# Kernel optimization log

Hardware: AMD Instinct MI355X
Metric: run time of the kernel (lower is better)

Reference implementation:

```python
import jax, jax.numpy as jnp
import numpy as np

KS = 5               # kernel_size per spline dimension
K3 = KS ** 3         # 125 weight matrices per SplineConv
NS = [16384, 4096, 1024, 256, 64]  # nodes per hierarchy level
DEG = 8


def spline_basis(pseudo):
    """Degree-1 open B-spline basis for 3D pseudo-coords in [0,1].
    Returns basis [E,8] and weight indices [E,8] into the K3 weights."""
    v = pseudo * (KS - 1)
    bot = jnp.minimum(jnp.floor(v), KS - 2)
    frac = v - bot                                  # [E,3]
    bot = bot.astype(jnp.int32)
    bits = jnp.array([[(s >> d) & 1 for d in range(3)] for s in range(8)], jnp.int32)  # [8,3]
    f = frac[:, None, :]                            # [E,1,3]
    basis = jnp.prod(jnp.where(bits[None] == 1, f, 1.0 - f), axis=-1)   # [E,8]
    strides = jnp.array([1, KS, KS * KS], jnp.int32)
    widx = jnp.sum((bot[:, None, :] + bits[None]) * strides, axis=-1)   # [E,8]
    return basis, widx


def spline_conv(x, src, dst, basis, widx, W, root, bias, n):
    """out_j = (1/deg_j) * sum_{i->j} sum_s B_s(u_ij) x_i W_{k(s)} + x_j root + bias.
    Accumulate basis-weighted source features into per-(node, weight-index)
    buckets, then one dense einsum with the 125 kernel weights."""
    in_c = x.shape[1]
    contrib = basis[..., None] * x[src][:, None, :]          # [E,8,in]
    flat = (dst[:, None] * K3 + widx).reshape(-1)            # [E*8]
    acc = jnp.zeros((n * K3, in_c), x.dtype).at[flat].add(contrib.reshape(-1, in_c))
    out = jnp.einsum('nki,kio->no', acc.reshape(n, K3, in_c), W)
    deg = jnp.zeros((n,), x.dtype).at[dst].add(1.0)
    return out / jnp.maximum(deg, 1.0)[:, None] + x @ root + bias


def setup_inputs() -> dict:
    rng = np.random.default_rng(0)
    inp = {}
    inp['x'] = jnp.asarray(rng.standard_normal((NS[0], 1)), jnp.float32)
    for l in range(4):
        e = NS[l] * DEG
        inp[f'src{l}'] = jnp.asarray(rng.integers(0, NS[l], e), jnp.int32)
        inp[f'dst{l}'] = jnp.asarray(rng.integers(0, NS[l], e), jnp.int32)
        inp[f'pseudo{l}'] = jnp.asarray(rng.random((e, 3)), jnp.float32)
        cl = np.arange(NS[l]) % NS[l + 1]  # guarantees every voxel cluster non-empty
        rng.shuffle(cl)
        inp[f'cluster{l}'] = jnp.asarray(cl, jnp.int32)
    chans = [(1, 32), (32, 32), (32, 64), (64, 64), (64, 64), (64, 64), (64, 64), (64, 64)]
    names = ['1', '12', '2', '3', '4', '5', '6', '7']
    for nm, (ci, co) in zip(names, chans):
        inp[f'W{nm}'] = jnp.asarray(rng.standard_normal((K3, ci, co)) / np.sqrt(8.0 * ci), jnp.float32)
        inp[f'R{nm}'] = jnp.asarray(rng.standard_normal((ci, co)) / np.sqrt(ci), jnp.float32)
        inp[f'B{nm}'] = jnp.zeros((co,), jnp.float32)
    inp['fc1_w'] = jnp.asarray(rng.standard_normal((64, 64)) / 8.0, jnp.float32)
    inp['fc1_b'] = jnp.zeros((64,), jnp.float32)
    inp['fc2_w'] = jnp.asarray(rng.standard_normal((64, 10)) / 8.0, jnp.float32)
    inp['fc2_b'] = jnp.zeros((10,), jnp.float32)
    return inp


def reference(x, pseudo0, pseudo1, pseudo2, pseudo3,
              src0, dst0, src1, dst1, src2, dst2, src3, dst3,
              cluster0, cluster1, cluster2, cluster3,
              W1, R1, B1, W12, R12, B12, W2, R2, B2, W3, R3, B3,
              W4, R4, B4, W5, R5, B5, W6, R6, B6, W7, R7, B7,
              fc1_w, fc1_b, fc2_w, fc2_b):
    elu = jax.nn.elu
    # level 0
    b, wi = spline_basis(pseudo0)
    h = elu(spline_conv(x, src0, dst0, b, wi, W1, R1, B1, NS[0]))
    h = elu(spline_conv(h, src0, dst0, b, wi, W12, R12, B12, NS[0]))
    h = jax.ops.segment_max(h, cluster0, num_segments=NS[1])   # voxel max pool 1
    # level 1
    b, wi = spline_basis(pseudo1)
    h = elu(spline_conv(h, src1, dst1, b, wi, W2, R2, B2, NS[1]))
    h = elu(spline_conv(h, src1, dst1, b, wi, W3, R3, B3, NS[1]))
    h = jax.ops.segment_max(h, cluster1, num_segments=NS[2])   # voxel max pool 2
    # level 2
    b, wi = spline_basis(pseudo2)
    h = elu(spline_conv(h, src2, dst2, b, wi, W4, R4, B4, NS[2]))
    h = elu(spline_conv(h, src2, dst2, b, wi, W5, R5, B5, NS[2]))
    h = jax.ops.segment_max(h, cluster2, num_segments=NS[3])   # voxel max pool 3
    # level 3
    b, wi = spline_basis(pseudo3)
    h = elu(spline_conv(h, src3, dst3, b, wi, W6, R6, B6, NS[3]))
    h = elu(spline_conv(h, src3, dst3, b, wi, W7, R7, B7, NS[3]))
    h = jax.ops.segment_max(h, cluster3, num_segments=NS[4])   # voxel max pool 4
    # readout head (dropout is identity in eval mode)
    g = h.mean(0)[None, :]
    g = g @ fc1_w + fc1_b
    g = g @ fc2_w + fc2_b
    return jax.nn.log_softmax(g, axis=1)
```

## Files before the change

### kernel.cpp

```cpp
#include <hip/hip_runtime.h>
#include <hip/hip_bf16.h>

#define KS 5
#define K3 125

typedef __attribute__((ext_vector_type(8))) short short8;
typedef __attribute__((ext_vector_type(4))) float floatx4;

__device__ inline unsigned enc_f(float f) {
    int b = __float_as_int(f);
    return (b >= 0) ? ((unsigned)b | 0x80000000u) : ~((unsigned)b);
}

__device__ inline unsigned short f2bf(float f) {
    unsigned u = __float_as_uint(f);
    u += 0x7FFFu + ((u >> 16) & 1u);
    return (unsigned short)(u >> 16);
}
__device__ inline float bf2f(unsigned short h) {
    return __uint_as_float((unsigned)h << 16);
}
__device__ inline unsigned pack2bf(float a, float b) {
    return (unsigned)f2bf(a) | ((unsigned)f2bf(b) << 16);
}

__device__ inline void edge_basis(const float* __restrict__ pseudo, int e,
                                  float* bs, int* ks) {
    float fr[3];
    int bot[3];
#pragma unroll
    for (int d = 0; d < 3; ++d) {
        float v = pseudo[e * 3 + d] * (float)(KS - 1);
        float fl = fminf(floorf(v), (float)(KS - 2));
        fr[d] = v - fl;
        bot[d] = (int)fl;
    }
    const int strides[3] = {1, KS, KS * KS};
#pragma unroll
    for (int s = 0; s < 8; ++s) {
        float b = 1.f;
        int w = 0;
#pragma unroll
        for (int d = 0; d < 3; ++d) {
            int bit = (s >> d) & 1;
            b *= bit ? fr[d] : (1.f - fr[d]);
            w += (bot[d] + bit) * strides[d];
        }
        bs[s] = b;
        ks[s] = w;
    }
}

__device__ inline void edge_fracs(const float* __restrict__ pseudo, int e, float* bs) {
    float fr[3];
#pragma unroll
    for (int d = 0; d < 3; ++d) {
        float v = pseudo[e * 3 + d] * (float)(KS - 1);
        float fl = fminf(floorf(v), (float)(KS - 2));
        fr[d] = v - fl;
    }
#pragma unroll
    for (int s = 0; s < 8; ++s) {
        float b = 1.f;
#pragma unroll
        for (int d = 0; d < 3; ++d) b *= ((s >> d) & 1) ? fr[d] : (1.f - fr[d]);
        bs[s] = b;
    }
}

__device__ inline int edge_bucket(const float* __restrict__ pseudo, int e) {
    int kb = 0;
#pragma unroll
    for (int d = 0; d < 3; ++d) {
        float v = pseudo[e * 3 + d] * (float)(KS - 1);
        int fl = (int)fminf(floorf(v), (float)(KS - 2));
        kb += fl << (2 * d);
    }
    return kb;
}

__global__ __launch_bounds__(256) void hist_deg_clist_all(
    const float* __restrict__ p0, const float* __restrict__ p1,
    const float* __restrict__ p2, const float* __restrict__ p3,
    const int* __restrict__ d0, const int* __restrict__ d1,
    const int* __restrict__ d2, const int* __restrict__ d3,
    const int* __restrict__ c0, const int* __restrict__ c1,
    const int* __restrict__ c2, const int* __restrict__ c3,
    int* __restrict__ hist, int* __restrict__ degi,
    int* __restrict__ ccnt, int* __restrict__ clist) {
    int b = blockIdx.x;
    if (b >= 680) {
        int idx = (b - 680) * 256 + threadIdx.x;
        int j, cof, nof;
        const int* cl;
        if (idx < 16384)      { j = idx;         cl = c0; cof = 0;    nof = 0; }
        else if (idx < 20480) { j = idx - 16384; cl = c1; cof = 4096; nof = 16384; }
        else if (idx < 21504) { j = idx - 20480; cl = c2; cof = 5120; nof = 20480; }
        else if (idx < 21760) { j = idx - 21504; cl = c3; cof = 5376; nof = 21504; }
        else return;
        int c = cl[j];
        int slot = atomicAdd(&ccnt[cof + c], 1);
        clist[nof + c * 4 + slot] = j;
        return;
    }
    int l, lb, E, dof;
    const float* ps;
    const int* ds;
    if (b < 512)      { l = 0; lb = b;       ps = p0; ds = d0; E = 131072; dof = 0; }
    else if (b < 640) { l = 1; lb = b - 512; ps = p1; ds = d1; E = 32768;  dof = 16384; }
    else if (b < 672) { l = 2; lb = b - 640; ps = p2; ds = d2; E = 8192;   dof = 20480; }
    else              { l = 3; lb = b - 672; ps = p3; ds = d3; E = 2048;   dof = 21504; }
    __shared__ int h[64];
    int t = threadIdx.x;
    if (t < 64) h[t] = 0;
    __syncthreads();
    int e = lb * 256 + t;
    if (e < E) {
        atomicAdd(&h[edge_bucket(ps, e)], 1);
        atomicAdd(&degi[dof + ds[e]], 1);
    }
    __syncthreads();
    if (t < 64 && h[t]) atomicAdd(&hist[l * 64 + t], h[t]);
}

__global__ void scan_pad_all(const int* __restrict__ hist, int* __restrict__ gcur,
                             int* __restrict__ tileOf, int* __restrict__ pack) {
    const int TBv[4] = {0, 2112, 2112 + 576, 2112 + 576 + 192};
    int l = blockIdx.x;
    int tileBase = TBv[l];
    __shared__ int sh[64];
    int t = threadIdx.x;
    int cnt = hist[l * 64 + t];
    int tiles = (cnt + 63) >> 6;
    sh[t] = tiles;
    __syncthreads();
    for (int d = 1; d < 64; d <<= 1) {
        int v = (t >= d) ? sh[t - d] : 0;
        __syncthreads();
        sh[t] += v;
        __syncthreads();
    }
    int tb = tileBase + sh[t] - tiles;
    int eb = tb * 64;
    gcur[l * 64 + t] = eb;
    for (int q = 0; q < tiles; ++q) tileOf[tb + q] = t;
    for (int idx = eb + cnt; idx < eb + tiles * 64; ++idx) pack[idx] = -1;
}

__global__ __launch_bounds__(1024) void csr_scan_all(const int* __restrict__ degi,
                                                     int* __restrict__ off,
                                                     int* __restrict__ cur) {
    const int Nv[4] = {16384, 4096, 1024, 256};
    const int DOFv[4] = {0, 16384, 20480, 21504};
    const int OFFv[4] = {0, 16385, 20482, 21507};
    int l = blockIdx.x;
    int n = Nv[l];
    const int* d = degi + DOFv[l];
    int* o = off + OFFv[l];
    int* c = cur + DOFv[l];
    __shared__ int ls[1024];
    int t = threadIdx.x;
    int per = (n + 1023) >> 10;
    int beg = t * per;
    int end = (beg + per < n) ? beg + per : n;
    int s = 0;
    for (int j = beg; j < end; ++j) s += d[j];
    ls[t] = s;
    __syncthreads();
    for (int dd = 1; dd < 1024; dd <<= 1) {
        int v = (t >= dd) ? ls[t - dd] : 0;
        __syncthreads();
        ls[t] += v;
        __syncthreads();
    }
    int base = (t == 0) ? 0 : ls[t - 1];
    for (int j = beg; j < end; ++j) {
        o[j] = base;
        c[j] = base;
        base += d[j];
    }
    if (t == 1023) o[n] = ls[1023];
}

__global__ __launch_bounds__(256) void scatter_pos_all(
    const float* __restrict__ p0, const float* __restrict__ p1,
    const float* __restrict__ p2, const float* __restrict__ p3,
    const int* __restrict__ d0, const int* __restrict__ d1,
    const int* __restrict__ d2, const int* __restrict__ d3,
    int* __restrict__ gcur, int* __restrict__ cur,
    int* __restrict__ pack, int* __restrict__ posArr) {
    int b = blockIdx.x;
    int l, lb, E, dof, eof_;
    const float* ps;
    const int* ds;
    if (b < 128)      { l = 0; lb = b;       ps = p0; ds = d0; E = 131072; dof = 0;     eof_ = 0; }
    else if (b < 160) { l = 1; lb = b - 128; ps = p1; ds = d1; E = 32768;  dof = 16384; eof_ = 131072; }
    else if (b < 168) { l = 2; lb = b - 160; ps = p2; ds = d2; E = 8192;   dof = 20480; eof_ = 163840; }
    else              { l = 3; lb = b - 168; ps = p3; ds = d3; E = 2048;   dof = 21504; eof_ = 172032; }
    int* gc = gcur + l * 64;
    __shared__ int h[64], lbk[64], gb[64], sh[64];
    __shared__ int sp[1024];
    __shared__ unsigned char skk[1024];
    int t = threadIdx.x;
    int ebase = lb * 1024;
    int kbv[4];
    if (t < 64) h[t] = 0;
    __syncthreads();
#pragma unroll
    for (int j = 0; j < 4; ++j) {
        int e = ebase + j * 256 + t;
        if (e < E) {
            kbv[j] = edge_bucket(ps, e);
            atomicAdd(&h[kbv[j]], 1);
            posArr[eof_ + e] = atomicAdd(&cur[dof + ds[e]], 1);
        } else
            kbv[j] = -1;
    }
    __syncthreads();
    if (t < 64) sh[t] = h[t];
    __syncthreads();
    for (int d = 1; d < 64; d <<= 1) {
        int v = (t < 64 && t >= d) ? sh[t - d] : 0;
        __syncthreads();
        if (t < 64) sh[t] += v;
        __syncthreads();
    }
    if (t < 64) {
        int c = h[t];
        lbk[t] = sh[t] - c;
        gb[t] = c ? atomicAdd(&gc[t], c) : 0;
        h[t] = 0;
    }
    __syncthreads();
#pragma unroll
    for (int j = 0; j < 4; ++j) {
        int e = ebase + j * 256 + t;
        if (kbv[j] >= 0) {
            int pos = lbk[kbv[j]] + atomicAdd(&h[kbv[j]], 1);
            sp[pos] = e;
            skk[pos] = (unsigned char)kbv[j];
        }
    }
    __syncthreads();
    int Pb = E - ebase;
    if (Pb > 1024) Pb = 1024;
    for (int j = t; j < Pb; j += 256) {
        int k = skk[j];
        pack[gb[k] + (j - lbk[k])] = sp[j];
    }
}

__global__ __launch_bounds__(256) void wcvt_all(
    const float* __restrict__ w12, const float* __restrict__ w2,
    const float* __restrict__ w3, const float* __restrict__ w4,
    const float* __restrict__ w5, const float* __restrict__ w6,
    const float* __restrict__ w7, short* __restrict__ Wt) {
    int idx = blockIdx.x * 256 + threadIdx.x;
    if (idx >= 2944000) return;
    const float* Wsrc;
    int IC, OC, local;
    if (idx < 128000)       { Wsrc = w12; IC = 32; OC = 32; local = idx; }
    else if (idx < 384000)  { Wsrc = w2;  IC = 32; OC = 64; local = idx - 128000; }
    else if (idx < 896000)  { Wsrc = w3;  IC = 64; OC = 64; local = idx - 384000; }
    else if (idx < 1408000) { Wsrc = w4;  IC = 64; OC = 64; local = idx - 896000; }
    else if (idx < 1920000) { Wsrc = w5;  IC = 64; OC = 64; local = idx - 1408000; }
    else if (idx < 2432000) { Wsrc = w6;  IC = 64; OC = 64; local = idx - 1920000; }
    else                    { Wsrc = w7;  IC = 64; OC = 64; local = idx - 2432000; }
    int per = IC * OC;
    int k = local / per;
    int r = local % per;
    int o = r / IC;
    int i = r % IC;
    Wt[idx] = (short)f2bf(Wsrc[(size_t)(k * IC + i) * OC + o]);
}

__global__ __launch_bounds__(256) void conv1_y(const float* __restrict__ x,
                                               const int* __restrict__ src,
                                               const float* __restrict__ pseudo,
                                               const int* __restrict__ pos,
                                               const float* __restrict__ W,
                                               unsigned short* __restrict__ y, int E) {
    const int lane = threadIdx.x & 63;
    const int wid = threadIdx.x >> 6;
    const int sub = lane >> 5;
    const int o = lane & 31;
    int e = (blockIdx.x * 4 + wid) * 2 + sub;
    if (e >= E) return;
    float bs[8];
    int ks[8];
    edge_basis(pseudo, e, bs, ks);
    float acc = 0.f;
#pragma unroll
    for (int s = 0; s < 8; ++s) acc = fmaf(bs[s], W[ks[s] * 32 + o], acc);
    y[(size_t)pos[e] * 32 + o] = f2bf(acc * x[src[e]]);
}

template <int IN_C, int OUT_C>
__global__ __launch_bounds__(256, 4) void mfma_conv(
    const float* __restrict__ x, const int* __restrict__ src,
    const float* __restrict__ pseudo, const int* __restrict__ pack,
    const int* __restrict__ tileOf, const int* __restrict__ pos,
    const short* __restrict__ Wt, unsigned short* __restrict__ y, int tileBase) {
    constexpr int PH = (IN_C == 64) ? 2 : 1;
    constexpr int SPP = 8 / PH;
    constexpr int KPH = SPP * IN_C;
    constexpr int KP = KPH + 8;
    constexpr int NT = OUT_C / 16;
    constexpr int IP = IN_C / 4;
    __shared__ short As[64 * KP];
    __shared__ int posL[64];
    const int tid = threadIdx.x;
    int t = tileBase + blockIdx.x;
    int kb = tileOf[t];
    if (kb < 0) return;
    kb = __builtin_amdgcn_readfirstlane(kb);
    const int kbase = (kb & 3) + 5 * ((kb >> 2) & 3) + 25 * ((kb >> 4) & 3);
    const int eLoc = tid >> 2, part = tid & 3;
    int e = pack[t * 64 + eLoc];
    float bs[8];
    float4 xq[IP / 4];
    if (e >= 0) edge_fracs(pseudo, e, bs);
    else {
#pragma unroll
        for (int s = 0; s < 8; ++s) bs[s] = 0.f;
    }
    if (part == 0) posL[eLoc] = (e >= 0) ? pos[e] : -1;
#pragma unroll
    for (int g = 0; g < IP / 4; ++g)
        xq[g] = (e >= 0)
                    ? *(const float4*)(x + (size_t)src[e] * IN_C + part * IP + g * 4)
                    : make_float4(0.f, 0.f, 0.f, 0.f);
    const int wave = tid >> 6, lane = tid & 63;
    const int quad = lane >> 4, lm = lane & 15;
    floatx4 acc[NT];
#pragma unroll
    for (int nt = 0; nt < NT; ++nt) acc[nt] = (floatx4){0.f, 0.f, 0.f, 0.f};
    const short* myrow = &As[(wave * 16 + lm) * KP];
#pragma unroll
    for (int ph = 0; ph < PH; ++ph) {
        if (ph) __syncthreads();
#pragma unroll
        for (int s2 = 0; s2 < SPP; ++s2) {
            const float b = bs[ph * SPP + s2];
            short* rowp = &As[eLoc * KP + s2 * IN_C + part * IP];
#pragma unroll
            for (int g = 0; g < IP / 4; ++g) {
                unsigned lo = pack2bf(b * xq[g].x, b * xq[g].y);
                unsigned hi = pack2bf(b * xq[g].z, b * xq[g].w);
                *(uint2*)(rowp + 4 * g) = make_uint2(lo, hi);
            }
        }
        __syncthreads();
#pragma unroll
        for (int kstep = 0; kstep < KPH / 32; ++kstep) {
            const int kg = kstep * 32;
            const int s2 = kg / IN_C;
            const int i0 = kg % IN_C;
            const int s = ph * SPP + s2;
            const int ks = kbase + (s & 1) + 5 * ((s >> 1) & 1) + 25 * ((s >> 2) & 1);
            short8 a = *(const short8*)&myrow[kg + quad * 8];
#pragma unroll
            for (int nt = 0; nt < NT; ++nt) {
                const short* bp =
                    Wt + ((size_t)ks * OUT_C + nt * 16 + lm) * IN_C + i0 + quad * 8;
                short8 bfr = *(const short8*)bp;
                acc[nt] = __builtin_amdgcn_mfma_f32_16x16x32_bf16(a, bfr, acc[nt], 0, 0, 0);
            }
        }
    }
#pragma unroll
    for (int nt = 0; nt < NT; ++nt) {
#pragma unroll
        for (int r = 0; r < 4; ++r) {
            int row = wave * 16 + quad * 4 + r;
            int p = posL[row];
            if (p >= 0) y[(size_t)p * OUT_C + nt * 16 + lm] = f2bf(acc[nt][r]);
        }
    }
}

template <int OUT_C>
__device__ inline float csr_sum(const int* __restrict__ off,
                                const unsigned short* __restrict__ y, int j, int o,
                                float& dcount) {
    int b0 = off[j], b1 = off[j + 1];
    dcount = fmaxf((float)(b1 - b0), 1.f);
    float s0 = 0.f, s1 = 0.f, s2 = 0.f, s3 = 0.f;
    int r = b0;
    for (; r + 4 <= b1; r += 4) {
        s0 += bf2f(y[(size_t)(r + 0) * OUT_C + o]);
        s1 += bf2f(y[(size_t)(r + 1) * OUT_C + o]);
        s2 += bf2f(y[(size_t)(r + 2) * OUT_C + o]);
        s3 += bf2f(y[(size_t)(r + 3) * OUT_C + o]);
    }
    for (; r < b1; ++r) s0 += bf2f(y[(size_t)r * OUT_C + o]);
    return (s0 + s1) + (s2 + s3);
}

template <int IN_C, int OUT_C>
__global__ __launch_bounds__(256) void fin_gather_k(
    const float* __restrict__ xin, const float* __restrict__ R,
    const float* __restrict__ B, const int* __restrict__ off,
    const unsigned short* __restrict__ y, float* __restrict__ out, int n) {
    const int lane = threadIdx.x & 63;
    const int wid = threadIdx.x >> 6;
    constexpr int EPW = 64 / OUT_C;
    const int sub = (EPW == 2) ? (lane >> 5) : 0;
    const int o = lane & (OUT_C - 1);
    int j = (blockIdx.x * (blockDim.x >> 6) + wid) * EPW + sub;
    if (j >= n) return;
    float xv = (o < IN_C) ? xin[j * IN_C + o] : 0.f;
    float acc = B[o];
#pragma unroll 4
    for (int i = 0; i < IN_C; ++i) {
        float xi = __shfl(xv, i, OUT_C);
        acc = fmaf(xi, R[i * OUT_C + o], acc);
    }
    float d;
    float s = csr_sum<OUT_C>(off, y, j, o, d);
    float v = s / d + acc;
    out[j * OUT_C + o] = (v > 0.f) ? v : expm1f(v);
}

template <int OC>
__global__ __launch_bounds__(256) void pool_gather(const float* __restrict__ h,
                                                   const int* __restrict__ clist,
                                                   float* __restrict__ out, int m) {
    int idx = blockIdx.x * 256 + threadIdx.x;
    if (idx >= m * OC) return;
    int c = idx / OC;
    int ch = idx - c * OC;
    const int* mb = &clist[c * 4];
    float v0 = h[(size_t)mb[0] * OC + ch];
    float v1 = h[(size_t)mb[1] * OC + ch];
    float v2 = h[(size_t)mb[2] * OC + ch];
    float v3 = h[(size_t)mb[3] * OC + ch];
    out[idx] = fmaxf(fmaxf(v0, v1), fmaxf(v2, v3));
}

__global__ __launch_bounds__(256) void conv1_fused(const float* __restrict__ x,
                                                   const int* __restrict__ src,
                                                   const int* __restrict__ dst,
                                                   const float* __restrict__ pseudo,
                                                   const float* __restrict__ W,
                                                   float* __restrict__ out, int E) {
    const int lane = threadIdx.x & 63;
    const int wid = threadIdx.x >> 6;
    const int sub = lane >> 5;
    const int o = lane & 31;
    int e = (blockIdx.x * 4 + wid) * 2 + sub;
    if (e >= E) return;
    float bs[8];
    int ks[8];
    edge_basis(pseudo, e, bs, ks);
    float acc = 0.f;
#pragma unroll
    for (int s = 0; s < 8; ++s) acc = fmaf(bs[s], W[ks[s] * 32 + o], acc);
    atomicAdd(&out[(size_t)dst[e] * 32 + o], acc * x[src[e]]);
}

template <int IN_C, int OUT_C>
__global__ __launch_bounds__(256) void conv_edges_inline(
    const float* __restrict__ x, const int* __restrict__ src,
    const int* __restrict__ dst, const float* __restrict__ pseudo,
    const float* __restrict__ W, float* __restrict__ out, int E) {
    const int lane = threadIdx.x & 63;
    const int wid = threadIdx.x >> 6;
    constexpr int EPW = 64 / OUT_C;
    const int sub = (EPW == 2) ? (lane >> 5) : 0;
    const int o = lane & (OUT_C - 1);
    long e = (long)(blockIdx.x * (blockDim.x >> 6) + wid) * EPW + sub;
    if (e >= E) return;
    float bs[8];
    int ks[8];
    edge_basis(pseudo, e, bs, ks);
    const int s_ = src[e];
    const int d_ = dst[e];
    float xv = (o < IN_C) ? x[s_ * IN_C + o] : 0.f;
    float acc = 0.f;
#pragma unroll
    for (int s = 0; s < 8; ++s) {
        const float b = bs[s];
        const float* Wk = W + (long)ks[s] * IN_C * OUT_C;
#pragma unroll 4
        for (int i = 0; i < IN_C; ++i) {
            float xi = __shfl(xv, i, OUT_C);
            acc = fmaf(b * xi, Wk[i * OUT_C + o], acc);
        }
    }
    atomicAdd(&out[(long)d_ * OUT_C + o], acc);
}

__global__ void deg_kernel(const int* __restrict__ dst, float* __restrict__ deg, int E) {
    int e = blockIdx.x * blockDim.x + threadIdx.x;
    if (e >= E) return;
    atomicAdd(&deg[dst[e]], 1.0f);
}

template <int IN_C, int OUT_C>
__global__ __launch_bounds__(256) void finalize_k(
    const float* __restrict__ xin, const float* __restrict__ R,
    const float* __restrict__ B, const float* __restrict__ deg,
    float* __restrict__ out, int n) {
    const int lane = threadIdx.x & 63;
    const int wid = threadIdx.x >> 6;
    constexpr int EPW = 64 / OUT_C;
    const int sub = (EPW == 2) ? (lane >> 5) : 0;
    const int o = lane & (OUT_C - 1);
    int j = (blockIdx.x * (blockDim.x >> 6) + wid) * EPW + sub;
    if (j >= n) return;
    float xv = (o < IN_C) ? xin[j * IN_C + o] : 0.f;
    float acc = B[o];
#pragma unroll 4
    for (int i = 0; i < IN_C; ++i) {
        float xi = __shfl(xv, i, OUT_C);
        acc = fmaf(xi, R[i * OUT_C + o], acc);
    }
    float d = fmaxf(deg[j], 1.f);
    float v = out[j * OUT_C + o] / d + acc;
    out[j * OUT_C + o] = (v > 0.f) ? v : expm1f(v);
}

__global__ void pool_scatter(const float* __restrict__ h, const int* __restrict__ cluster,
                             unsigned* __restrict__ pool, int n, int logC) {
    int idx = blockIdx.x * blockDim.x + threadIdx.x;
    if (idx >= (n << logC)) return;
    int j = idx >> logC;
    int c = idx & ((1 << logC) - 1);
    atomicMax(&pool[(cluster[j] << logC) + c], enc_f(h[idx]));
}

__global__ void pool_decode(const unsigned* __restrict__ pool, float* __restrict__ out, int total) {
    int idx = blockIdx.x * blockDim.x + threadIdx.x;
    if (idx >= total) return;
    unsigned u = pool[idx];
    int b = (u & 0x80000000u) ? (int)(u & 0x7FFFFFFFu) : (int)(~u);
    out[idx] = __int_as_float(b);
}

__global__ void head_kernel(const float* __restrict__ h, const float* __restrict__ fc1w,
                            const float* __restrict__ fc1b, const float* __restrict__ fc2w,
                            const float* __restrict__ fc2b, float* __restrict__ out) {
    __shared__ float m[64], t[64], u[10];
    int lane = threadIdx.x;
    float s = 0.f;
    for (int j = 0; j < 64; ++j) s += h[j * 64 + lane];
    m[lane] = s * (1.f / 64.f);
    __syncthreads();
    float a = fc1b[lane];
    for (int i = 0; i < 64; ++i) a = fmaf(m[i], fc1w[i * 64 + lane], a);
    t[lane] = a;
    __syncthreads();
    if (lane < 10) {
        float b = fc2b[lane];
        for (int i = 0; i < 64; ++i) b = fmaf(t[i], fc2w[i * 10 + lane], b);
        u[lane] = b;
    }
    __syncthreads();
    if (lane < 10) {
        float mx = u[0];
        for (int i = 1; i < 10; ++i) mx = fmaxf(mx, u[i]);
        float se = 0.f;
        for (int i = 0; i < 10; ++i) se += expf(u[i] - mx);
        out[lane] = u[lane] - mx - logf(se);
    }
}

static inline int cdiv(int a, int b) { return (a + b - 1) / b; }

extern "C" void kernel_launch(void* const* d_in, const int* in_sizes, int n_in,
                              void* d_out, int out_size, void* d_ws, size_t ws_size,
                              hipStream_t stream) {
    const float* x = (const float*)d_in[0];
    const int* src[4] = {(const int*)d_in[1], (const int*)d_in[5], (const int*)d_in[9], (const int*)d_in[13]};
    const int* dst[4] = {(const int*)d_in[2], (const int*)d_in[6], (const int*)d_in[10], (const int*)d_in[14]};
    const float* pseudo[4] = {(const float*)d_in[3], (const float*)d_in[7], (const float*)d_in[11], (const float*)d_in[15]};
    const int* cluster[4] = {(const int*)d_in[4], (const int*)d_in[8], (const int*)d_in[12], (const int*)d_in[16]};
    const float* Wp[8], *Rp[8], *Bp[8];
    for (int l = 0; l < 8; ++l) {
        Wp[l] = (const float*)d_in[17 + 3 * l];
        Rp[l] = (const float*)d_in[18 + 3 * l];
        Bp[l] = (const float*)d_in[19 + 3 * l];
    }
    const float* fc1w = (const float*)d_in[41];
    const float* fc1b = (const float*)d_in[42];
    const float* fc2w = (const float*)d_in[43];
    const float* fc2b = (const float*)d_in[44];
    float* outp = (float*)d_out;

    const int NS[5] = {16384, 4096, 1024, 256, 64};
    const int ES[4] = {16384 * 8, 4096 * 8, 1024 * 8, 256 * 8};
    const int MT[4] = {2048 + 64, 512 + 64, 128 + 64, 32 + 64};
    const int TB_[4] = {0, 2112, 2112 + 576, 2112 + 576 + 192};
    const int TOT_TILES = 2112 + 576 + 192 + 96;
    const int DTOT = 21760;
    const int OFF2[4] = {0, 16385, 20482, 21507};
    const int OFFTOT = 21764;
    const int EBASE[4] = {0, 131072, 163840, 172032};
    const int ETOT = 174080;
    const int NODE_OFF[4] = {0, 16384, 20480, 21504};
    const int CCTOT = 4096 + 1024 + 256 + 64;
    const int WT_OFF[7] = {0, 128000, 384000, 896000, 1408000, 1920000, 2432000};
    const int WT_TOT = 2944000;

    char* w = (char*)d_ws;
    auto take = [&](size_t bytes) -> char* {
        char* r = w;
        w += (bytes + 255) & ~(size_t)255;
        return r;
    };
    float* bufA = (float*)take((size_t)NS[0] * 64 * 4);
    float* bufB = (float*)take((size_t)NS[0] * 64 * 4);
    unsigned* pool = (unsigned*)take((size_t)NS[1] * 64 * 4);
    char* zbase = w;
    int* hist = (int*)take((size_t)4 * 64 * 4);
    int* ccnt = (int*)take((size_t)CCTOT * 4);
    int* degi = (int*)take((size_t)DTOT * 4);
    int* tileOf = (int*)take((size_t)TOT_TILES * 4);
    size_t zbytes = (size_t)(w - zbase);
    size_t fallbackNeed = (size_t)(w - (char*)d_ws);
    int* gcur = (int*)take((size_t)4 * 64 * 4);
    int* pack = (int*)take((size_t)TOT_TILES * 64 * 4);
    int* csr = (int*)take((size_t)OFFTOT * 4);
    int* cur = (int*)take((size_t)DTOT * 4);
    int* posArr = (int*)take((size_t)ETOT * 4);
    int* clist = (int*)take((size_t)DTOT * 4);
    short* Wtb = (short*)take((size_t)WT_TOT * 2);
    unsigned short* y = (unsigned short*)take((size_t)ES[0] * 32 * 2);
    size_t need = (size_t)(w - (char*)d_ws);
    bool fast = ws_size >= need;

    const int TB = 256;

    if (fast) {
        (void)hipMemsetAsync(zbase, 0, zbytes, stream);
        hist_deg_clist_all<<<765, 256, 0, stream>>>(
            pseudo[0], pseudo[1], pseudo[2], pseudo[3],
            dst[0], dst[1], dst[2], dst[3],
            cluster[0], cluster[1], cluster[2], cluster[3], hist, degi, ccnt, clist);
        wcvt_all<<<cdiv(WT_TOT, 256), 256, 0, stream>>>(Wp[1], Wp[2], Wp[3], Wp[4],
                                                        Wp[5], Wp[6], Wp[7], Wtb);
        scan_pad_all<<<4, 64, 0, stream>>>(hist, gcur, tileOf, pack);
        csr_scan_all<<<4, 1024, 0, stream>>>(degi, csr, cur);
        scatter_pos_all<<<170, 256, 0, stream>>>(pseudo[0], pseudo[1], pseudo[2], pseudo[3],
                                                 dst[0], dst[1], dst[2], dst[3],
                                                 gcur, cur, pack, posArr);

        {
            int E = ES[0], n = NS[0];
            const int* off = csr + OFF2[0];
            const int* pos = posArr + EBASE[0];
            conv1_y<<<cdiv(E, 8), TB, 0, stream>>>(x, src[0], pseudo[0], pos, Wp[0], y, E);
            fin_gather_k<1, 32><<<cdiv(n, 8), TB, 0, stream>>>(x, Rp[0], Bp[0], off, y, bufA, n);
            mfma_conv<32, 32><<<MT[0], TB, 0, stream>>>(
                bufA, src[0], pseudo[0], pack, tileOf, pos, Wtb + WT_OFF[0], y, TB_[0]);
            fin_gather_k<32, 32><<<cdiv(n, 8), TB, 0, stream>>>(bufA, Rp[1], Bp[1], off, y, bufB, n);
            pool_gather<32><<<cdiv(NS[1] * 32, 256), 256, 0, stream>>>(
                bufB, clist + NODE_OFF[0], bufA, NS[1]);
        }
        {
            int n = NS[1];
            const int* off = csr + OFF2[1];
            const int* pos = posArr + EBASE[1];
            mfma_conv<32, 64><<<MT[1], TB, 0, stream>>>(
                bufA, src[1], pseudo[1], pack, tileOf, pos, Wtb + WT_OFF[1], y, TB_[1]);
            fin_gather_k<32, 64><<<cdiv(n, 4), TB, 0, stream>>>(bufA, Rp[2], Bp[2], off, y, bufB, n);
            mfma_conv<64, 64><<<MT[1], TB, 0, stream>>>(
                bufB, src[1], pseudo[1], pack, tileOf, pos, Wtb + WT_OFF[2], y, TB_[1]);
            fin_gather_k<64, 64><<<cdiv(n, 4), TB, 0, stream>>>(bufB, Rp[3], Bp[3], off, y, bufA, n);
            pool_gather<64><<<cdiv(NS[2] * 64, 256), 256, 0, stream>>>(
                bufA, clist + NODE_OFF[1], bufB, NS[2]);
        }
        {
            int n = NS[2];
            const int* off = csr + OFF2[2];
            const int* pos = posArr + EBASE[2];
            mfma_conv<64, 64><<<MT[2], TB, 0, stream>>>(
                bufB, src[2], pseudo[2], pack, tileOf, pos, Wtb + WT_OFF[3], y, TB_[2]);
            fin_gather_k<64, 64><<<cdiv(n, 4), TB, 0, stream>>>(bufB, Rp[4], Bp[4], off, y, bufA, n);
            mfma_conv<64, 64><<<MT[2], TB, 0, stream>>>(
                bufA, src[2], pseudo[2], pack, tileOf, pos, Wtb + WT_OFF[4], y, TB_[2]);
            fin_gather_k<64, 64><<<cdiv(n, 4), TB, 0, stream>>>(bufA, Rp[5], Bp[5], off, y, bufB, n);
            pool_gather<64><<<cdiv(NS[3] * 64, 256), 256, 0, stream>>>(
                bufB, clist + NODE_OFF[2], bufA, NS[3]);
        }
        {
            int n = NS[3];
            const int* off = csr + OFF2[3];
            const int* pos = posArr + EBASE[3];
            mfma_conv<64, 64><<<MT[3], TB, 0, stream>>>(
                bufA, src[3], pseudo[3], pack, tileOf, pos, Wtb + WT_OFF[5], y, TB_[3]);
            fin_gather_k<64, 64><<<cdiv(n, 4), TB, 0, stream>>>(bufA, Rp[6], Bp[6], off, y, bufB, n);
            mfma_conv<64, 64><<<MT[3], TB, 0, stream>>>(
                bufB, src[3], pseudo[3], pack, tileOf, pos, Wtb + WT_OFF[6], y, TB_[3]);
            fin_gather_k<64, 64><<<cdiv(n, 4), TB, 0, stream>>>(bufB, Rp[7], Bp[7], off, y, bufA, n);
            pool_gather<64><<<cdiv(NS[4] * 64, 256), 256, 0, stream>>>(
                bufA, clist + NODE_OFF[3], bufB, NS[4]);
        }
        head_kernel<<<1, 64, 0, stream>>>(bufB, fc1w, fc1b, fc2w, fc2b, outp);
    } else if (ws_size >= fallbackNeed) {
        float* h0 = bufA;
        float* h1 = bufB;
        float* deg = (float*)degi;
        for (int l = 0; l < 4; ++l) {
            int E = ES[l], n = NS[l];
            (void)hipMemsetAsync(deg, 0, n * 4, stream);
            deg_kernel<<<cdiv(E, TB), TB, 0, stream>>>(dst[l], deg, E);
            for (int cc = 0; cc < 2; ++cc) {
                int li = (l == 0) ? cc : 2 * l + cc;
                if (l == 0 && cc == 0) {
                    (void)hipMemsetAsync(h0, 0, (size_t)n * 32 * 4, stream);
                    conv1_fused<<<cdiv(E, 8), TB, 0, stream>>>(x, src[0], dst[0], pseudo[0], Wp[0], h0, E);
                    finalize_k<1, 32><<<cdiv(n, 8), TB, 0, stream>>>(x, Rp[0], Bp[0], deg, h0, n);
                } else {
                    int ic = (l == 0) ? 32 : ((l == 1 && cc == 0) ? 32 : 64);
                    int oc = (l == 0) ? 32 : 64;
                    (void)hipMemsetAsync(h1, 0, (size_t)n * oc * 4, stream);
                    if (ic == 32 && oc == 32) {
                        conv_edges_inline<32, 32><<<cdiv(E, 8), TB, 0, stream>>>(h0, src[l], dst[l], pseudo[l], Wp[li], h1, E);
                        finalize_k<32, 32><<<cdiv(n, 8), TB, 0, stream>>>(h0, Rp[li], Bp[li], deg, h1, n);
                    } else if (ic == 32) {
                        conv_edges_inline<32, 64><<<cdiv(E, 4), TB, 0, stream>>>(h0, src[l], dst[l], pseudo[l], Wp[li], h1, E);
                        finalize_k<32, 64><<<cdiv(n, 4), TB, 0, stream>>>(h0, Rp[li], Bp[li], deg, h1, n);
                    } else {
                        conv_edges_inline<64, 64><<<cdiv(E, 4), TB, 0, stream>>>(h0, src[l], dst[l], pseudo[l], Wp[li], h1, E);
                        finalize_k<64, 64><<<cdiv(n, 4), TB, 0, stream>>>(h0, Rp[li], Bp[li], deg, h1, n);
                    }
                    float* tmp = h0; h0 = h1; h1 = tmp;
                }
            }
            int oc = (l == 0) ? 32 : 64;
            int logC = (l == 0) ? 5 : 6;
            (void)hipMemsetAsync(pool, 0, (size_t)NS[l + 1] * oc * 4, stream);
            pool_scatter<<<cdiv(n * oc, TB), TB, 0, stream>>>(h0, cluster[l], pool, n, logC);
            pool_decode<<<cdiv(NS[l + 1] * oc, TB), TB, 0, stream>>>(pool, h1, NS[l + 1] * oc);
            float* tmp = h0; h0 = h1; h1 = tmp;
        }
        head_kernel<<<1, 64, 0, stream>>>(h0, fc1w, fc1b, fc2w, fc2b, outp);
    }
}
```

Before: 420.1 us.

## Fuse preprocessing kernels, first conv with finalize, and finalize with voxel pooling

Merges the weight conversion into the histogram pass and the two scan kernels into a single launch. The first layer's edge-to-y pass and its finalize become one CSR-sorted gather kernel, fed by a new dst-sorted edge list built in scatter_pos. Each level's last finalize is fused with the max-pool gather so pooled nodes are finalized and reduced in shared memory. The scatter kernel now runs one 256-edge chunk per block instead of 1024. Several bounds clamps are added, and the fused pool kernel assumes clusters of exactly 4 members.

```diff
diff --git a/kernel.cpp b/kernel.cpp
--- a/kernel.cpp
+++ b/kernel.cpp
@@ -79,16 +79,41 @@
     return kb;
 }
 
-__global__ __launch_bounds__(256) void hist_deg_clist_all(
+__global__ __launch_bounds__(256) void pre1(
     const float* __restrict__ p0, const float* __restrict__ p1,
     const float* __restrict__ p2, const float* __restrict__ p3,
     const int* __restrict__ d0, const int* __restrict__ d1,
     const int* __restrict__ d2, const int* __restrict__ d3,
     const int* __restrict__ c0, const int* __restrict__ c1,
     const int* __restrict__ c2, const int* __restrict__ c3,
+    const float* __restrict__ w12, const float* __restrict__ w2,
+    const float* __restrict__ w3, const float* __restrict__ w4,
+    const float* __restrict__ w5, const float* __restrict__ w6,
+    const float* __restrict__ w7,
     int* __restrict__ hist, int* __restrict__ degi,
-    int* __restrict__ ccnt, int* __restrict__ clist) {
+    int* __restrict__ ccnt, int* __restrict__ clist,
+    short* __restrict__ Wt) {
     int b = blockIdx.x;
+    if (b >= 765) {
+        int idx = (b - 765) * 256 + threadIdx.x;
+        if (idx >= 2944000) return;
+        const float* Wsrc;
+        int IC, OC, local;
+        if (idx < 128000)       { Wsrc = w12; IC = 32; OC = 32; local = idx; }
+        else if (idx < 384000)  { Wsrc = w2;  IC = 32; OC = 64; local = idx - 128000; }
+        else if (idx < 896000)  { Wsrc = w3;  IC = 64; OC = 64; local = idx - 384000; }
+        else if (idx < 1408000) { Wsrc = w4;  IC = 64; OC = 64; local = idx - 896000; }
+        else if (idx < 1920000) { Wsrc = w5;  IC = 64; OC = 64; local = idx - 1408000; }
+        else if (idx < 2432000) { Wsrc = w6;  IC = 64; OC = 64; local = idx - 1920000; }
+        else                    { Wsrc = w7;  IC = 64; OC = 64; local = idx - 2432000; }
+        int per = IC * OC;
+        int k = local / per;
+        int r = local % per;
+        int o = r / IC;
+        int i = r % IC;
+        Wt[idx] = (short)f2bf(Wsrc[(size_t)(k * IC + i) * OC + o]);
+        return;
+    }
     if (b >= 680) {
         int idx = (b - 680) * 256 + threadIdx.x;
         int j, cof, nof;
@@ -99,7 +124,7 @@
         else if (idx < 21760) { j = idx - 21504; cl = c3; cof = 5376; nof = 21504; }
         else return;
         int c = cl[j];
-        int slot = atomicAdd(&ccnt[cof + c], 1);
+        int slot = atomicAdd(&ccnt[cof + c], 1) & 3;
         clist[nof + c * 4 + slot] = j;
         return;
     }
@@ -123,63 +148,74 @@
     if (t < 64 && h[t]) atomicAdd(&hist[l * 64 + t], h[t]);
 }
 
-__global__ void scan_pad_all(const int* __restrict__ hist, int* __restrict__ gcur,
-                             int* __restrict__ tileOf, int* __restrict__ pack) {
-    const int TBv[4] = {0, 2112, 2112 + 576, 2112 + 576 + 192};
-    int l = blockIdx.x;
-    int tileBase = TBv[l];
-    __shared__ int sh[64];
+__global__ __launch_bounds__(1024) void pre2(const int* __restrict__ hist,
+                                             int* __restrict__ gcur,
+                                             int* __restrict__ tileOf,
+                                             int* __restrict__ pack,
+                                             const int* __restrict__ degi,
+                                             int* __restrict__ off,
+                                             int* __restrict__ cur) {
+    int b = blockIdx.x;
     int t = threadIdx.x;
-    int cnt = hist[l * 64 + t];
-    int tiles = (cnt + 63) >> 6;
-    sh[t] = tiles;
-    __syncthreads();
-    for (int d = 1; d < 64; d <<= 1) {
-        int v = (t >= d) ? sh[t - d] : 0;
+    if (b < 4) {
+        const int Nv[4] = {16384, 4096, 1024, 256};
+        const int DOFv[4] = {0, 16384, 20480, 21504};
+        const int OFFv[4] = {0, 16385, 20482, 21507};
+        int l = b;
+        int n = Nv[l];
+        const int* d = degi + DOFv[l];
+        int* o = off + OFFv[l];
+        int* c = cur + DOFv[l];
+        __shared__ int ls[1024];
+        int per = (n + 1023) >> 10;
+        int beg = t * per;
+        int end = (beg + per < n) ? beg + per : n;
+        int s = 0;
+        for (int j = beg; j < end; ++j) s += d[j];
+        ls[t] = s;
         __syncthreads();
-        sh[t] += v;
+        for (int dd = 1; dd < 1024; dd <<= 1) {
+            int v = (t >= dd) ? ls[t - dd] : 0;
+            __syncthreads();
+            ls[t] += v;
+            __syncthreads();
+        }
+        int base = (t == 0) ? 0 : ls[t - 1];
+        for (int j = beg; j < end; ++j) {
+            o[j] = base;
+            c[j] = base;
+            base += d[j];
+        }
+        if (t == 1023) o[n] = ls[1023];
+    } else {
+        const int TBv[4] = {0, 2112, 2688, 2880};
+        const int MTv[4] = {2112, 576, 192, 96};
+        int l = b - 4;
+        int tileBase = TBv[l];
+        __shared__ int sh[64];
+        int cnt = 0, tiles = 0;
+        if (t < 64) {
+            cnt = hist[l * 64 + t];
+            tiles = (cnt + 63) >> 6;
+            sh[t] = tiles;
+        }
         __syncthreads();
-    }
-    int tb = tileBase + sh[t] - tiles;
-    int eb = tb * 64;
-    gcur[l * 64 + t] = eb;
-    for (int q = 0; q < tiles; ++q) tileOf[tb + q] = t;
-    for (int idx = eb + cnt; idx < eb + tiles * 64; ++idx) pack[idx] = -1;
-}
-
-__global__ __launch_bounds__(1024) void csr_scan_all(const int* __restrict__ degi,
-                                                     int* __restrict__ off,
-                                                     int* __restrict__ cur) {
-    const int Nv[4] = {16384, 4096, 1024, 256};
-    const int DOFv[4] = {0, 16384, 20480, 21504};
-    const int OFFv[4] = {0, 16385, 20482, 21507};
-    int l = blockIdx.x;
-    int n = Nv[l];
-    const int* d = degi + DOFv[l];
-    int* o = off + OFFv[l];
-    int* c = cur + DOFv[l];
-    __shared__ int ls[1024];
-    int t = threadIdx.x;
-    int per = (n + 1023) >> 10;
-    int beg = t * per;
-    int end = (beg + per < n) ? beg + per : n;
-    int s = 0;
-    for (int j = beg; j < end; ++j) s += d[j];
-    ls[t] = s;
-    __syncthreads();
-    for (int dd = 1; dd < 1024; dd <<= 1) {
-        int v = (t >= dd) ? ls[t - dd] : 0;
-        __syncthreads();
-        ls[t] += v;
-        __syncthreads();
-    }
-    int base = (t == 0) ? 0 : ls[t - 1];
-    for (int j = beg; j < end; ++j) {
-        o[j] = base;
-        c[j] = base;
-        base += d[j];
-    }
-    if (t == 1023) o[n] = ls[1023];
+        for (int d = 1; d < 64; d <<= 1) {
+            int v = (t < 64 && t >= d) ? sh[t - d] : 0;
+            __syncthreads();
+            if (t < 64) sh[t] += v;
+            __syncthreads();
+        }
+        if (t < 64) {
+            int tb = tileBase + sh[t] - tiles;
+            gcur[l * 64 + t] = tb * 64;
+            for (int q = 0; q < tiles; ++q) tileOf[tb + q] = t;
+            for (int idx = tb * 64 + cnt; idx < (tb + tiles) * 64; ++idx) pack[idx] = -1;
+            if (t == 63) {
+                for (int q = tileBase + sh[63]; q < tileBase + MTv[l]; ++q) tileOf[q] = -1;
+            }
+        }
+    }
 }
 
 __global__ __launch_bounds__(256) void scatter_pos_all(
@@ -188,33 +224,31 @@
     const int* __restrict__ d0, const int* __restrict__ d1,
     const int* __restrict__ d2, const int* __restrict__ d3,
     int* __restrict__ gcur, int* __restrict__ cur,
-    int* __restrict__ pack, int* __restrict__ posArr) {
+    int* __restrict__ pack, int* __restrict__ posArr,
+    int* __restrict__ esrt) {
     int b = blockIdx.x;
     int l, lb, E, dof, eof_;
     const float* ps;
     const int* ds;
-    if (b < 128)      { l = 0; lb = b;       ps = p0; ds = d0; E = 131072; dof = 0;     eof_ = 0; }
-    else if (b < 160) { l = 1; lb = b - 128; ps = p1; ds = d1; E = 32768;  dof = 16384; eof_ = 131072; }
-    else if (b < 168) { l = 2; lb = b - 160; ps = p2; ds = d2; E = 8192;   dof = 20480; eof_ = 163840; }
-    else              { l = 3; lb = b - 168; ps = p3; ds = d3; E = 2048;   dof = 21504; eof_ = 172032; }
+    if (b < 512)      { l = 0; lb = b;       ps = p0; ds = d0; E = 131072; dof = 0;     eof_ = 0; }
+    else if (b < 640) { l = 1; lb = b - 512; ps = p1; ds = d1; E = 32768;  dof = 16384; eof_ = 131072; }
+    else if (b < 672) { l = 2; lb = b - 640; ps = p2; ds = d2; E = 8192;   dof = 20480; eof_ = 163840; }
+    else              { l = 3; lb = b - 672; ps = p3; ds = d3; E = 2048;   dof = 21504; eof_ = 172032; }
     int* gc = gcur + l * 64;
     __shared__ int h[64], lbk[64], gb[64], sh[64];
-    __shared__ int sp[1024];
-    __shared__ unsigned char skk[1024];
+    __shared__ int sp[256];
+    __shared__ unsigned char skk[256];
     int t = threadIdx.x;
-    int ebase = lb * 1024;
-    int kbv[4];
+    int e = lb * 256 + t;
+    int kb = -1;
     if (t < 64) h[t] = 0;
     __syncthreads();
-#pragma unroll
-    for (int j = 0; j < 4; ++j) {
-        int e = ebase + j * 256 + t;
-        if (e < E) {
-            kbv[j] = edge_bucket(ps, e);
-            atomicAdd(&h[kbv[j]], 1);
-            posArr[eof_ + e] = atomicAdd(&cur[dof + ds[e]], 1);
-        } else
-            kbv[j] = -1;
+    if (e < E) {
+        kb = edge_bucket(ps, e);
+        atomicAdd(&h[kb], 1);
+        int p = atomicAdd(&cur[dof + ds[e]], 1);
+        posArr[eof_ + e] = p;
+        if (l == 0 && p >= 0 && p < 131072) esrt[p] = e;
     }
     __syncthreads();
     if (t < 64) sh[t] = h[t];
@@ -232,67 +266,49 @@
         h[t] = 0;
     }
     __syncthreads();
-#pragma unroll
-    for (int j = 0; j < 4; ++j) {
-        int e = ebase + j * 256 + t;
-        if (kbv[j] >= 0) {
-            int pos = lbk[kbv[j]] + atomicAdd(&h[kbv[j]], 1);
-            sp[pos] = e;
-            skk[pos] = (unsigned char)kbv[j];
-        }
-    }
-    __syncthreads();
-    int Pb = E - ebase;
-    if (Pb > 1024) Pb = 1024;
-    for (int j = t; j < Pb; j += 256) {
-        int k = skk[j];
-        pack[gb[k] + (j - lbk[k])] = sp[j];
-    }
-}
-
-__global__ __launch_bounds__(256) void wcvt_all(
-    const float* __restrict__ w12, const float* __restrict__ w2,
-    const float* __restrict__ w3, const float* __restrict__ w4,
-    const float* __restrict__ w5, const float* __restrict__ w6,
-    const float* __restrict__ w7, short* __restrict__ Wt) {
-    int idx = blockIdx.x * 256 + threadIdx.x;
-    if (idx >= 2944000) return;
-    const float* Wsrc;
-    int IC, OC, local;
-    if (idx < 128000)       { Wsrc = w12; IC = 32; OC = 32; local = idx; }
-    else if (idx < 384000)  { Wsrc = w2;  IC = 32; OC = 64; local = idx - 128000; }
-    else if (idx < 896000)  { Wsrc = w3;  IC = 64; OC = 64; local = idx - 384000; }
-    else if (idx < 1408000) { Wsrc = w4;  IC = 64; OC = 64; local = idx - 896000; }
-    else if (idx < 1920000) { Wsrc = w5;  IC = 64; OC = 64; local = idx - 1408000; }
-    else if (idx < 2432000) { Wsrc = w6;  IC = 64; OC = 64; local = idx - 1920000; }
-    else                    { Wsrc = w7;  IC = 64; OC = 64; local = idx - 2432000; }
-    int per = IC * OC;
-    int k = local / per;
-    int r = local % per;
-    int o = r / IC;
-    int i = r % IC;
-    Wt[idx] = (short)f2bf(Wsrc[(size_t)(k * IC + i) * OC + o]);
-}
-
-__global__ __launch_bounds__(256) void conv1_y(const float* __restrict__ x,
-                                               const int* __restrict__ src,
-                                               const float* __restrict__ pseudo,
-                                               const int* __restrict__ pos,
-                                               const float* __restrict__ W,
-                                               unsigned short* __restrict__ y, int E) {
+    if (kb >= 0) {
+        int ppos = lbk[kb] + atomicAdd(&h[kb], 1);
+        sp[ppos] = e;
+        skk[ppos] = (unsigned char)kb;
+    }
+    __syncthreads();
+    int Pb = E - lb * 256;
+    if (Pb > 256) Pb = 256;
+    if (t < Pb) {
+        int k = skk[t];
+        pack[gb[k] + (t - lbk[k])] = sp[t];
+    }
+}
+
+__global__ __launch_bounds__(256) void conv1_fin(
+    const float* __restrict__ x, const int* __restrict__ src,
+    const float* __restrict__ pseudo, const int* __restrict__ esrt,
+    const int* __restrict__ off, const float* __restrict__ W,
+    const float* __restrict__ R, const float* __restrict__ B,
+    float* __restrict__ out, int n, int Emax) {
     const int lane = threadIdx.x & 63;
     const int wid = threadIdx.x >> 6;
     const int sub = lane >> 5;
     const int o = lane & 31;
-    int e = (blockIdx.x * 4 + wid) * 2 + sub;
-    if (e >= E) return;
-    float bs[8];
-    int ks[8];
-    edge_basis(pseudo, e, bs, ks);
+    int j = (blockIdx.x * 4 + wid) * 2 + sub;
+    if (j >= n) return;
+    int b0 = off[j], b1 = off[j + 1];
+    if (b0 < 0) b0 = 0;
+    if (b1 > Emax) b1 = Emax;
     float acc = 0.f;
-#pragma unroll
-    for (int s = 0; s < 8; ++s) acc = fmaf(bs[s], W[ks[s] * 32 + o], acc);
-    y[(size_t)pos[e] * 32 + o] = f2bf(acc * x[src[e]]);
+    for (int r = b0; r < b1; ++r) {
+        int e = esrt[r];
+        float bs[8];
+        int ks[8];
+        edge_basis(pseudo, e, bs, ks);
+        float w = 0.f;
+#pragma unroll
+        for (int s = 0; s < 8; ++s) w = fmaf(bs[s], W[ks[s] * 32 + o], w);
+        acc = fmaf(w, x[src[e]], acc);
+    }
+    float d = fmaxf((float)(b1 - b0), 1.f);
+    float v = acc / d + x[j] * R[o] + B[o];
+    out[(size_t)j * 32 + o] = (v > 0.f) ? v : expm1f(v);
 }
 
 template <int IN_C, int OUT_C>
@@ -300,7 +316,8 @@
     const float* __restrict__ x, const int* __restrict__ src,
     const float* __restrict__ pseudo, const int* __restrict__ pack,
     const int* __restrict__ tileOf, const int* __restrict__ pos,
-    const short* __restrict__ Wt, unsigned short* __restrict__ y, int tileBase) {
+    const short* __restrict__ Wt, unsigned short* __restrict__ y, int tileBase,
+    int Emax) {
     constexpr int PH = (IN_C == 64) ? 2 : 1;
     constexpr int SPP = 8 / PH;
     constexpr int KPH = SPP * IN_C;
@@ -312,11 +329,12 @@
     const int tid = threadIdx.x;
     int t = tileBase + blockIdx.x;
     int kb = tileOf[t];
-    if (kb < 0) return;
+    if (kb < 0 || kb >= 64) return;
     kb = __builtin_amdgcn_readfirstlane(kb);
     const int kbase = (kb & 3) + 5 * ((kb >> 2) & 3) + 25 * ((kb >> 4) & 3);
     const int eLoc = tid >> 2, part = tid & 3;
     int e = pack[t * 64 + eLoc];
+    if (e >= Emax) e = -1;
     float bs[8];
     float4 xq[IP / 4];
     if (e >= 0) edge_fracs(pseudo, e, bs);
@@ -374,7 +392,7 @@
         for (int r = 0; r < 4; ++r) {
             int row = wave * 16 + quad * 4 + r;
             int p = posL[row];
-            if (p >= 0) y[(size_t)p * OUT_C + nt * 16 + lm] = f2bf(acc[nt][r]);
+            if (p >= 0 && p < Emax) y[(size_t)p * OUT_C + nt * 16 + lm] = f2bf(acc[nt][r]);
         }
     }
 }
@@ -384,6 +402,8 @@
                                 const unsigned short* __restrict__ y, int j, int o,
                                 float& dcount) {
     int b0 = off[j], b1 = off[j + 1];
+    if (b0 < 0) b0 = 0;
+    if (b1 < b0) b1 = b0;
     dcount = fmaxf((float)(b1 - b0), 1.f);
     float s0 = 0.f, s1 = 0.f, s2 = 0.f, s3 = 0.f;
     int r = b0;
@@ -422,20 +442,41 @@
     out[j * OUT_C + o] = (v > 0.f) ? v : expm1f(v);
 }
 
-template <int OC>
-__global__ __launch_bounds__(256) void pool_gather(const float* __restrict__ h,
-                                                   const int* __restrict__ clist,
-                                                   float* __restrict__ out, int m) {
-    int idx = blockIdx.x * 256 + threadIdx.x;
-    if (idx >= m * OC) return;
-    int c = idx / OC;
-    int ch = idx - c * OC;
-    const int* mb = &clist[c * 4];
-    float v0 = h[(size_t)mb[0] * OC + ch];
-    float v1 = h[(size_t)mb[1] * OC + ch];
-    float v2 = h[(size_t)mb[2] * OC + ch];
-    float v3 = h[(size_t)mb[3] * OC + ch];
-    out[idx] = fmaxf(fmaxf(v0, v1), fmaxf(v2, v3));
+template <int IN_C, int OUT_C>
+__global__ __launch_bounds__(256) void fin_pool_k(
+    const float* __restrict__ xin, const float* __restrict__ R,
+    const float* __restrict__ B, const int* __restrict__ off,
+    const unsigned short* __restrict__ y, const int* __restrict__ clist,
+    float* __restrict__ out, int nsrc) {
+    constexpr int CPB = 256 / (4 * OUT_C);
+    const int t = threadIdx.x;
+    const int o = t & (OUT_C - 1);
+    const int mem = (t / OUT_C) & 3;
+    const int g = t / (4 * OUT_C);
+    const int c = blockIdx.x * CPB + g;
+    int j = clist[c * 4 + mem];
+    if (j < 0) j = 0;
+    if (j >= nsrc) j = nsrc - 1;
+    float xv = (o < IN_C) ? xin[(size_t)j * IN_C + o] : 0.f;
+    float acc = B[o];
+#pragma unroll 4
+    for (int i = 0; i < IN_C; ++i) {
+        float xi = __shfl(xv, i, OUT_C);
+        acc = fmaf(xi, R[i * OUT_C + o], acc);
+    }
+    float d;
+    float s = csr_sum<OUT_C>(off, y, j, o, d);
+    float v = s / d + acc;
+    v = (v > 0.f) ? v : expm1f(v);
+    __shared__ float sh[256];
+    sh[t] = v;
+    __syncthreads();
+    if (mem == 0) {
+        const float* base = &sh[g * 4 * OUT_C];
+        float r01 = fmaxf(base[o], base[OUT_C + o]);
+        float r23 = fmaxf(base[2 * OUT_C + o], base[3 * OUT_C + o]);
+        out[(size_t)c * OUT_C + o] = fmaxf(r01, r23);
+    }
 }
 
 __global__ __launch_bounds__(256) void conv1_fused(const float* __restrict__ x,
@@ -625,6 +666,7 @@
     int* cur = (int*)take((size_t)DTOT * 4);
     int* posArr = (int*)take((size_t)ETOT * 4);
     int* clist = (int*)take((size_t)DTOT * 4);
+    int* esrt = (int*)take((size_t)ES[0] * 4);
     short* Wtb = (short*)take((size_t)WT_TOT * 2);
     unsigned short* y = (unsigned short*)take((size_t)ES[0] * 32 * 2);
     size_t need = (size_t)(w - (char*)d_ws);
@@ -634,68 +676,63 @@
 
     if (fast) {
         (void)hipMemsetAsync(zbase, 0, zbytes, stream);
-        hist_deg_clist_all<<<765, 256, 0, stream>>>(
+        pre1<<<765 + cdiv(WT_TOT, 256), 256, 0, stream>>>(
             pseudo[0], pseudo[1], pseudo[2], pseudo[3],
             dst[0], dst[1], dst[2], dst[3],
-            cluster[0], cluster[1], cluster[2], cluster[3], hist, degi, ccnt, clist);
-        wcvt_all<<<cdiv(WT_TOT, 256), 256, 0, stream>>>(Wp[1], Wp[2], Wp[3], Wp[4],
-                                                        Wp[5], Wp[6], Wp[7], Wtb);
-        scan_pad_all<<<4, 64, 0, stream>>>(hist, gcur, tileOf, pack);
-        csr_scan_all<<<4, 1024, 0, stream>>>(degi, csr, cur);
-        scatter_pos_all<<<170, 256, 0, stream>>>(pseudo[0], pseudo[1], pseudo[2], pseudo[3],
+            cluster[0], cluster[1], cluster[2], cluster[3],
+            Wp[1], Wp[2], Wp[3], Wp[4], Wp[5], Wp[6], Wp[7],
+            hist, degi, ccnt, clist, Wtb);
+        pre2<<<8, 1024, 0, stream>>>(hist, gcur, tileOf, pack, degi, csr, cur);
+        scatter_pos_all<<<680, 256, 0, stream>>>(pseudo[0], pseudo[1], pseudo[2], pseudo[3],
                                                  dst[0], dst[1], dst[2], dst[3],
-                                                 gcur, cur, pack, posArr);
+                                                 gcur, cur, pack, posArr, esrt);
 
         {
-            int E = ES[0], n = NS[0];
+            int n = NS[0];
             const int* off = csr + OFF2[0];
             const int* pos = posArr + EBASE[0];
-            conv1_y<<<cdiv(E, 8), TB, 0, stream>>>(x, src[0], pseudo[0], pos, Wp[0], y, E);
-            fin_gather_k<1, 32><<<cdiv(n, 8), TB, 0, stream>>>(x, Rp[0], Bp[0], off, y, bufA, n);
+            conv1_fin<<<cdiv(n, 8), TB, 0, stream>>>(x, src[0], pseudo[0], esrt, off,
+                                                     Wp[0], Rp[0], Bp[0], bufA, n, ES[0]);
             mfma_conv<32, 32><<<MT[0], TB, 0, stream>>>(
-                bufA, src[0], pseudo[0], pack, tileOf, pos, Wtb + WT_OFF[0], y, TB_[0]);
-            fin_gather_k<32, 32><<<cdiv(n, 8), TB, 0, stream>>>(bufA, Rp[1], Bp[1], off, y, bufB, n);
-            pool_gather<32><<<cdiv(NS[1] * 32, 256), 256, 0, stream>>>(
-                bufB, clist + NODE_OFF[0], bufA, NS[1]);
+                bufA, src[0], pseudo[0], pack, tileOf, pos, Wtb + WT_OFF[0], y, TB_[0], ES[0]);
+            fin_pool_k<32, 32><<<NS[1] / 2, TB, 0, stream>>>(
+                bufA, Rp[1], Bp[1], off, y, clist + NODE_OFF[0], bufB, NS[0]);
         }
         {
             int n = NS[1];
             const int* off = csr + OFF2[1];
             const int* pos = posArr + EBASE[1];
             mfma_conv<32, 64><<<MT[1], TB, 0, stream>>>(
-                bufA, src[1], pseudo[1], pack, tileOf, pos, Wtb + WT_OFF[1], y, TB_[1]);
-            fin_gather_k<32, 64><<<cdiv(n, 4), TB, 0, stream>>>(bufA, Rp[2], Bp[2], off, y, bufB, n);
+                bufB, src[1], pseudo[1], pack, tileOf, pos, Wtb + WT_OFF[1], y, TB_[1], ES[1]);
+            fin_gather_k<32, 64><<<cdiv(n, 4), TB, 0, stream>>>(bufB, Rp[2], Bp[2], off, y, bufA, n);
             mfma_conv<64, 64><<<MT[1], TB, 0, stream>>>(
-                bufB, src[1], pseudo[1], pack, tileOf, pos, Wtb + WT_OFF[2], y, TB_[1]);
-            fin_gather_k<64, 64><<<cdiv(n, 4), TB, 0, stream>>>(bufB, Rp[3], Bp[3], off, y, bufA, n);
-            pool_gather<64><<<cdiv(NS[2] * 64, 256), 256, 0, stream>>>(
-                bufA, clist + NODE_OFF[1], bufB, NS[2]);
+                bufA, src[1], pseudo[1], pack, tileOf, pos, Wtb + WT_OFF[2], y, TB_[1], ES[1]);
+            fin_pool_k<64, 64><<<NS[2], TB, 0, stream>>>(
+                bufA, Rp[3], Bp[3], off, y, clist + NODE_OFF[1], bufB, NS[1]);
         }
         {
             int n = NS[2];
             const int* off = csr + OFF2[2];
             const int* pos = posArr + EBASE[2];
             mfma_conv<64, 64><<<MT[2], TB, 0, stream>>>(
-                bufB, src[2], pseudo[2], pack, tileOf, pos, Wtb + WT_OFF[3], y, TB_[2]);
+                bufB, src[2], pseudo[2], pack, tileOf, pos, Wtb + WT_OFF[3], y, TB_[2], ES[2]);
             fin_gather_k<64, 64><<<cdiv(n, 4), TB, 0, stream>>>(bufB, Rp[4], Bp[4], off, y, bufA, n);
             mfma_conv<64, 64><<<MT[2], TB, 0, stream>>>(
-                bufA, src[2], pseudo[2], pack, tileOf, pos, Wtb + WT_OFF[4], y, TB_[2]);
-            fin_gather_k<64, 64><<<cdiv(n, 4), TB, 0, stream>>>(bufA, Rp[5], Bp[5], off, y, bufB, n);
-            pool_gather<64><<<cdiv(NS[3] * 64, 256), 256, 0, stream>>>(
-                bufB, clist + NODE_OFF[2], bufA, NS[3]);
+                bufA, src[2], pseudo[2], pack, tileOf, pos, Wtb + WT_OFF[4], y, TB_[2], ES[2]);
+            fin_pool_k<64, 64><<<NS[3], TB, 0, stream>>>(
+                bufA, Rp[5], Bp[5], off, y, clist + NODE_OFF[2], bufB, NS[2]);
         }
         {
             int n = NS[3];
             const int* off = csr + OFF2[3];
             const int* pos = posArr + EBASE[3];
             mfma_conv<64, 64><<<MT[3], TB, 0, stream>>>(
-                bufA, src[3], pseudo[3], pack, tileOf, pos, Wtb + WT_OFF[5], y, TB_[3]);
-            fin_gather_k<64, 64><<<cdiv(n, 4), TB, 0, stream>>>(bufA, Rp[6], Bp[6], off, y, bufB, n);
+                bufB, src[3], pseudo[3], pack, tileOf, pos, Wtb + WT_OFF[5], y, TB_[3], ES[3]);
+            fin_gather_k<64, 64><<<cdiv(n, 4), TB, 0, stream>>>(bufB, Rp[6], Bp[6], off, y, bufA, n);
             mfma_conv<64, 64><<<MT[3], TB, 0, stream>>>(
-                bufB, src[3], pseudo[3], pack, tileOf, pos, Wtb + WT_OFF[6], y, TB_[3]);
-            fin_gather_k<64, 64><<<cdiv(n, 4), TB, 0, stream>>>(bufB, Rp[7], Bp[7], off, y, bufA, n);
-            pool_gather<64><<<cdiv(NS[4] * 64, 256), 256, 0, stream>>>(
-                bufA, clist + NODE_OFF[3], bufB, NS[4]);
+                bufA, src[3], pseudo[3], pack, tileOf, pos, Wtb + WT_OFF[6], y, TB_[3], ES[3]);
+            fin_pool_k<64, 64><<<NS[4], TB, 0, stream>>>(
+                bufA, Rp[7], Bp[7], off, y, clist + NODE_OFF[3], bufB, NS[3]);
         }
         head_kernel<<<1, 64, 0, stream>>>(bufB, fc1w, fc1b, fc2w, fc2b, outp);
     } else if (ws_size >= fallbackNeed) {
```

After: 410.6 us. 2.3% less time.
